# Optimization experiments

Measured on AMD Instinct MI355X. Metric: run time of the kernel, lower is better.

The kernel has to match this reference:

```python
import jax, jax.numpy as jnp
import numpy as np

N = 50000   # nodes
E = 640000  # edges (before self-loops)
D = 128     # in_channels = hidden_channels = out_channels
EPS_BN = 1e-5


def _gat(x, src, dst, W, a_src, a_dst, b, heads, concat):
    """PyG-style GATConv (self-loops already appended to src/dst)."""
    n = x.shape[0]
    C = W.shape[1] // heads
    xp = (x @ W).reshape(n, heads, C)                      # [N,H,C]
    asrc = jnp.sum(xp * a_src, -1)                          # [N,H]
    adst = jnp.sum(xp * a_dst, -1)                          # [N,H]
    e = jax.nn.leaky_relu(asrc[src] + adst[dst], 0.2)       # [Etot,H]
    m = jax.ops.segment_max(e, dst, num_segments=n)
    ex = jnp.exp(e - m[dst])
    s = jax.ops.segment_sum(ex, dst, num_segments=n)
    alpha = ex / (s[dst] + 1e-16)                           # segment softmax
    out = jax.ops.segment_sum(xp[src] * alpha[..., None], dst, num_segments=n)
    out = out.reshape(n, heads * C) if concat else out.mean(1)
    return out + b


def _gru(x, h, Wih, Whh, bih, bhh):
    gi = x @ Wih + bih
    gh = h @ Whh + bhh
    ir, iz, inn = jnp.split(gi, 3, -1)
    hr, hz, hn = jnp.split(gh, 3, -1)
    r = jax.nn.sigmoid(ir + hr)
    z = jax.nn.sigmoid(iz + hz)
    nn_ = jnp.tanh(inn + r * hn)
    return (1.0 - z) * nn_ + z * h


def setup_inputs() -> dict:
    key = jax.random.key(0)
    ks = jax.random.split(key, 32)
    f32 = jnp.float32
    p = lambda k, shape, s=0.1: jax.random.normal(k, shape, f32) * s
    inp = {
        "node_features": jax.random.normal(ks[0], (N, D), f32),
        "edge_index": jax.random.randint(ks[1], (2, E), 0, N),
        "x_prev1": jax.random.normal(ks[2], (N, D), f32),
        "x_prev2": jax.random.normal(ks[3], (N, D), f32),
        "ts": jax.random.uniform(ks[4], (N, 1), f32),
        # TimeEncode params
        "basis_freq": jnp.asarray(1.0 / 10 ** np.linspace(0, 9, D), f32),
        "phase": jnp.zeros((D,), f32),
        # MergeLayer: Linear(2D -> D)
        "merge_W": p(ks[5], (2 * D, D)),
        "merge_b": p(ks[6], (D,)),
        # layer1 GATConv(D -> D, heads=1, concat)
        "gat1_W": p(ks[7], (D, D)),
        "gat1_asrc": p(ks[8], (1, D)),
        "gat1_adst": p(ks[9], (1, D)),
        "gat1_b": p(ks[10], (D,)),
        # layer1 GRUCell(D, D)
        "gru1_Wih": p(ks[11], (D, 3 * D)),
        "gru1_Whh": p(ks[12], (D, 3 * D)),
        "gru1_bih": p(ks[13], (3 * D,)),
        "gru1_bhh": p(ks[14], (3 * D,)),
        # layer2 GATConv(D -> D, heads=1, concat=False)
        "gat2_W": p(ks[15], (D, D)),
        "gat2_asrc": p(ks[16], (1, D)),
        "gat2_adst": p(ks[17], (1, D)),
        "gat2_b": p(ks[18], (D,)),
        # layer2 GRUCell(D, D)
        "gru2_Wih": p(ks[19], (D, 3 * D)),
        "gru2_Whh": p(ks[20], (D, 3 * D)),
        "gru2_bih": p(ks[21], (3 * D,)),
        "gru2_bhh": p(ks[22], (3 * D,)),
        # skip connection Linear(D -> D)
        "skip_W": p(ks[23], (D, D)),
        "skip_b": p(ks[24], (D,)),
    }
    return inp


def reference(node_features, edge_index, x_prev1, x_prev2, ts,
              basis_freq, phase, merge_W, merge_b,
              gat1_W, gat1_asrc, gat1_adst, gat1_b,
              gru1_Wih, gru1_Whh, gru1_bih, gru1_bhh,
              gat2_W, gat2_asrc, gat2_adst, gat2_b,
              gru2_Wih, gru2_Whh, gru2_bih, gru2_bhh,
              skip_W, skip_b):
    n = node_features.shape[0]
    loop = jnp.arange(n)
    src = jnp.concatenate([edge_index[0], loop])  # add self-loops (PyG default)
    dst = jnp.concatenate([edge_index[1], loop])

    # TimeEncode: cos(ts * freq + phase) -> [N, D]
    t_embed = jnp.cos(ts * basis_freq[None, :] + phase[None, :])
    # MergeLayer
    x = jnp.concatenate([node_features, t_embed], -1) @ merge_W + merge_b

    # layer1: GAT + GRU, relu
    h1c = _gat(x, src, dst, gat1_W, gat1_asrc, gat1_adst, gat1_b, 1, True)
    H1 = jax.nn.relu(_gru(h1c, x_prev1, gru1_Wih, gru1_Whh, gru1_bih, gru1_bhh))

    # layer2: GAT + GRU + skip + fresh BatchNorm1d (training stats, identity affine)
    h2c = _gat(H1, src, dst, gat2_W, gat2_asrc, gat2_adst, gat2_b, 1, False)
    H2 = _gru(h2c, x_prev2, gru2_Wih, gru2_Whh, gru2_bih, gru2_bhh)
    H2 = H2 + (x @ skip_W + skip_b)
    mu = H2.mean(0)
    var = H2.var(0)
    H2 = (H2 - mu) / jnp.sqrt(var + EPS_BN)
    return (H1, H2)
```

## Files before the change

### kernel.cpp

```cpp
#include <hip/hip_runtime.h>
#include <math.h>

#define D 128
#define D3 384

typedef __attribute__((ext_vector_type(8))) short bf16x8;
typedef __attribute__((ext_vector_type(4))) float f32x4;
typedef __attribute__((ext_vector_type(4))) unsigned int u32x4;

__device__ __forceinline__ float fsigmoid(float x){
  return __builtin_amdgcn_rcpf(1.0f + __expf(-x));
}
__device__ __forceinline__ float ftanh(float x){
  float e = __expf(2.0f * x);
  return 1.0f - 2.0f * __builtin_amdgcn_rcpf(e + 1.0f);
}

__device__ __forceinline__ unsigned short f2bf(float f){
  unsigned u = __float_as_uint(f);
  return (unsigned short)((u + 0x7FFFu + ((u >> 16) & 1u)) >> 16);
}

__global__ __launch_bounds__(256) void k_init0(int* __restrict__ cnt, float* __restrict__ bns, int n){
  int idx = blockIdx.x * 256 + threadIdx.x;
  if (idx < n) cnt[idx] = 0;
  if (idx < 2 * D) bns[idx] = 0.0f;
}

__global__ __launch_bounds__(256) void k_wcvt(const float* __restrict__ W, unsigned short* __restrict__ Wt,
                                              int Nc, int K){
  int idx = blockIdx.x * 256 + threadIdx.x;
  if (idx >= K * Nc) return;
  int k = idx / Nc, c = idx - k * Nc;
  Wt[c * K + k] = f2bf(W[idx]);
}

__global__ __launch_bounds__(256) void k_merge(const float* __restrict__ nf, const float* __restrict__ ts,
                                               const float* __restrict__ freq, const float* __restrict__ phase,
                                               const unsigned short* __restrict__ Bt,
                                               const float* __restrict__ bias,
                                               unsigned short* __restrict__ xb, int M){
  __shared__ __align__(16) unsigned short Alds[64 * 256];
  const int tid = threadIdx.x;
  const int lane = tid & 63;
  const int w = tid >> 6;
  const int row0 = blockIdx.y * 64;

  #pragma unroll
  for (int r = 0; r < 8; ++r){
    int u = r * 256 + tid;
    int row = u >> 5, c16 = u & 31;
    int gr = row0 + row;
    union { unsigned short s[8]; bf16x8 v; } t;
    if (gr < M){
      if (c16 < 16){
        const float* p = nf + (size_t)gr * 128 + c16 * 8;
        float4 f0 = *(const float4*)p, f1 = *(const float4*)(p + 4);
        t.s[0]=f2bf(f0.x); t.s[1]=f2bf(f0.y); t.s[2]=f2bf(f0.z); t.s[3]=f2bf(f0.w);
        t.s[4]=f2bf(f1.x); t.s[5]=f2bf(f1.y); t.s[6]=f2bf(f1.z); t.s[7]=f2bf(f1.w);
      } else {
        float tv = ts[gr];
        int ch0 = (c16 - 16) * 8;
        float4 fq0 = *(const float4*)&freq[ch0],  fq1 = *(const float4*)&freq[ch0 + 4];
        float4 ph0 = *(const float4*)&phase[ch0], ph1 = *(const float4*)&phase[ch0 + 4];
        t.s[0]=f2bf(__cosf(tv*fq0.x+ph0.x)); t.s[1]=f2bf(__cosf(tv*fq0.y+ph0.y));
        t.s[2]=f2bf(__cosf(tv*fq0.z+ph0.z)); t.s[3]=f2bf(__cosf(tv*fq0.w+ph0.w));
        t.s[4]=f2bf(__cosf(tv*fq1.x+ph1.x)); t.s[5]=f2bf(__cosf(tv*fq1.y+ph1.y));
        t.s[6]=f2bf(__cosf(tv*fq1.z+ph1.z)); t.s[7]=f2bf(__cosf(tv*fq1.w+ph1.w));
      }
    } else {
      #pragma unroll
      for (int q = 0; q < 8; ++q) t.s[q] = 0;
    }
    int c16s = c16 ^ (row & 7);
    *(bf16x8*)&Alds[row * 256 + c16s * 8] = t.v;
  }
  __syncthreads();

  f32x4 acc[4][2];
  #pragma unroll
  for (int mf = 0; mf < 4; ++mf)
    #pragma unroll
    for (int nfi = 0; nfi < 2; ++nfi)
      #pragma unroll
      for (int i = 0; i < 4; ++i) acc[mf][nfi][i] = 0.0f;

  const int l15 = lane & 15, lg = lane >> 4;
  #pragma unroll
  for (int kk = 0; kk < 8; ++kk){
    const int c16 = kk * 4 + lg;
    bf16x8 a[4], b[2];
    #pragma unroll
    for (int nfi = 0; nfi < 2; ++nfi){
      int brow = w * 32 + nfi * 16 + l15;
      b[nfi] = *(const bf16x8*)&Bt[(size_t)brow * 256 + c16 * 8];
    }
    #pragma unroll
    for (int mf = 0; mf < 4; ++mf){
      int row = mf * 16 + l15;
      a[mf] = *(bf16x8*)&Alds[row * 256 + ((c16 ^ (row & 7))) * 8];
    }
    #pragma unroll
    for (int mf = 0; mf < 4; ++mf)
      #pragma unroll
      for (int nfi = 0; nfi < 2; ++nfi)
        acc[mf][nfi] = __builtin_amdgcn_mfma_f32_16x16x32_bf16(a[mf], b[nfi], acc[mf][nfi], 0, 0, 0);
  }

  #pragma unroll
  for (int nfi = 0; nfi < 2; ++nfi){
    int c = w * 32 + nfi * 16 + l15;
    float bv = bias[c];
    #pragma unroll
    for (int mf = 0; mf < 4; ++mf)
      #pragma unroll
      for (int i = 0; i < 4; ++i){
        int rr = row0 + mf * 16 + lg * 4 + i;
        if (rr < M) xb[(size_t)rr * 128 + c] = f2bf(acc[mf][nfi][i] + bv);
      }
  }
}

template<bool ABF16, bool OUTBF, bool ACCUM, bool BIAS>
__global__ __launch_bounds__(256) void k_mgemm(const void* __restrict__ Av,
                                               const unsigned short* __restrict__ Bt,
                                               const float* __restrict__ bias,
                                               void* __restrict__ Cv, int M, int Nc){
  __shared__ __align__(16) unsigned short Alds[64 * 128];
  const int tid = threadIdx.x;
  const int lane = tid & 63;
  const int w = tid >> 6;
  const int row0 = blockIdx.y * 64;
  const int col0 = blockIdx.x * 128;

  #pragma unroll
  for (int r = 0; r < 4; ++r){
    int u = r * 256 + tid;
    int row = u >> 4, c16 = u & 15;
    int gr = row0 + row;
    int c16s = c16 ^ (row & 7);
    if (ABF16){
      u32x4 v = {0,0,0,0};
      if (gr < M) v = *(const u32x4*)((const unsigned short*)Av + (size_t)gr * 128 + c16 * 8);
      *(u32x4*)&Alds[row * 128 + c16s * 8] = v;
    } else {
      float4 f0 = make_float4(0.f,0.f,0.f,0.f), f1 = f0;
      if (gr < M){
        const float* p = (const float*)Av + (size_t)gr * 128 + c16 * 8;
        f0 = *(const float4*)p; f1 = *(const float4*)(p + 4);
      }
      union { unsigned short s[8]; bf16x8 v; } t;
      t.s[0]=f2bf(f0.x); t.s[1]=f2bf(f0.y); t.s[2]=f2bf(f0.z); t.s[3]=f2bf(f0.w);
      t.s[4]=f2bf(f1.x); t.s[5]=f2bf(f1.y); t.s[6]=f2bf(f1.z); t.s[7]=f2bf(f1.w);
      *(bf16x8*)&Alds[row * 128 + c16s * 8] = t.v;
    }
  }
  __syncthreads();

  f32x4 acc[4][2];
  #pragma unroll
  for (int mf = 0; mf < 4; ++mf)
    #pragma unroll
    for (int nfi = 0; nfi < 2; ++nfi)
      #pragma unroll
      for (int i = 0; i < 4; ++i) acc[mf][nfi][i] = 0.0f;

  const int l15 = lane & 15, lg = lane >> 4;
  #pragma unroll
  for (int kk = 0; kk < 4; ++kk){
    const int c16 = kk * 4 + lg;
    bf16x8 a[4], b[2];
    #pragma unroll
    for (int nfi = 0; nfi < 2; ++nfi){
      int brow = col0 + w * 32 + nfi * 16 + l15;
      b[nfi] = *(const bf16x8*)&Bt[(size_t)brow * 128 + c16 * 8];
    }
    #pragma unroll
    for (int mf = 0; mf < 4; ++mf){
      int row = mf * 16 + l15;
      a[mf] = *(bf16x8*)&Alds[row * 128 + ((c16 ^ (row & 7))) * 8];
    }
    #pragma unroll
    for (int mf = 0; mf < 4; ++mf)
      #pragma unroll
      for (int nfi = 0; nfi < 2; ++nfi)
        acc[mf][nfi] = __builtin_amdgcn_mfma_f32_16x16x32_bf16(a[mf], b[nfi], acc[mf][nfi], 0, 0, 0);
  }

  #pragma unroll
  for (int nfi = 0; nfi < 2; ++nfi){
    int c = col0 + w * 32 + nfi * 16 + l15;
    float bv = BIAS ? bias[c] : 0.0f;
    #pragma unroll
    for (int mf = 0; mf < 4; ++mf)
      #pragma unroll
      for (int i = 0; i < 4; ++i){
        int rr = row0 + mf * 16 + lg * 4 + i;
        if (rr < M){
          size_t o = (size_t)rr * Nc + c;
          float v = acc[mf][nfi][i] + bv;
          if (OUTBF){
            ((unsigned short*)Cv)[o] = f2bf(v);
          } else {
            float* C = (float*)Cv;
            if (ACCUM) v += C[o];
            C[o] = v;
          }
        }
      }
  }
}

__global__ __launch_bounds__(256) void k_attn(const unsigned short* __restrict__ xpb,
                                              const float* __restrict__ a_s, const float* __restrict__ a_d,
                                              float* __restrict__ asrc, float* __restrict__ adst, int n){
  int wave = (blockIdx.x * 256 + threadIdx.x) >> 6;
  int lane = threadIdx.x & 63;
  if (wave >= n) return;
  unsigned u = *(const unsigned*)&xpb[(size_t)wave * D + 2 * lane];
  float lo = __uint_as_float(u << 16);
  float hi = __uint_as_float(u & 0xFFFF0000u);
  float2 as2 = *(const float2*)&a_s[2 * lane];
  float2 ad2 = *(const float2*)&a_d[2 * lane];
  float sa = lo * as2.x + hi * as2.y;
  float sd = lo * ad2.x + hi * ad2.y;
  #pragma unroll
  for (int off = 32; off > 0; off >>= 1){
    sa += __shfl_down(sa, off);
    sd += __shfl_down(sd, off);
  }
  if (lane == 0){ asrc[wave] = sa; adst[wave] = sd; }
}

__global__ __launch_bounds__(256) void k_hist(const int* __restrict__ ei, int* __restrict__ cnt, int e, int etot){
  int t = blockIdx.x * 256 + threadIdx.x;
  if (t >= etot) return;
  int d_ = (t < e) ? ei[e + t] : (t - e);
  atomicAdd(&cnt[d_], 1);
}

__global__ __launch_bounds__(256) void k_scan1(const int* __restrict__ cnt, int* __restrict__ off,
                                               int* __restrict__ bsum, int n){
  __shared__ int sm[256];
  int i = blockIdx.x * 256 + threadIdx.x;
  int v = (i < n) ? cnt[i] : 0;
  sm[threadIdx.x] = v;
  __syncthreads();
  #pragma unroll
  for (int d = 1; d < 256; d <<= 1){
    int t = (threadIdx.x >= d) ? sm[threadIdx.x - d] : 0;
    __syncthreads();
    sm[threadIdx.x] += t;
    __syncthreads();
  }
  if (i < n) off[i] = sm[threadIdx.x] - v;
  if (threadIdx.x == 255) bsum[blockIdx.x] = sm[255];
}

__global__ __launch_bounds__(256) void k_scan2(int* __restrict__ bsum, int nb){
  __shared__ int sm[256];
  int v = (threadIdx.x < nb) ? bsum[threadIdx.x] : 0;
  sm[threadIdx.x] = v;
  __syncthreads();
  #pragma unroll
  for (int d = 1; d < 256; d <<= 1){
    int t = (threadIdx.x >= d) ? sm[threadIdx.x - d] : 0;
    __syncthreads();
    sm[threadIdx.x] += t;
    __syncthreads();
  }
  if (threadIdx.x < nb) bsum[threadIdx.x] = sm[threadIdx.x] - v;
}

__global__ __launch_bounds__(256) void k_scan3(int* __restrict__ off, const int* __restrict__ bsum,
                                               int* __restrict__ cursor, int n, int etot){
  int i = blockIdx.x * 256 + threadIdx.x;
  if (i < n){
    int o = off[i] + bsum[blockIdx.x];
    off[i] = o;
    cursor[i] = o;
  }
  if (i == 0) off[n] = etot;
}

__global__ __launch_bounds__(256) void k_scatter(const int* __restrict__ ei, int* __restrict__ cursor,
                                                 int* __restrict__ csr, int e, int etot){
  int t = blockIdx.x * 256 + threadIdx.x;
  if (t >= etot) return;
  int s_, d_;
  if (t < e){ s_ = ei[t]; d_ = ei[e + t]; } else { s_ = d_ = t - e; }
  int pos = atomicAdd(&cursor[d_], 1);
  csr[pos] = s_;
}

__global__ __launch_bounds__(256) void k_gatconv(const int* __restrict__ off, const int* __restrict__ csr,
                                                 const float* __restrict__ asrc, const float* __restrict__ adst,
                                                 const unsigned short* __restrict__ xpb,
                                                 const float* __restrict__ bias,
                                                 unsigned short* __restrict__ outb, int n){
  int w = (blockIdx.x * 256 + threadIdx.x) >> 6;
  int lane = threadIdx.x & 63;
  if (w >= n) return;
  const int o0 = off[w], o1 = off[w + 1];
  const float ad = adst[w];
  float m = -1e30f;
  for (int j = o0 + lane; j < o1; j += 64){
    float v = asrc[csr[j]] + ad;
    v = (v > 0.0f) ? v : 0.2f * v;
    m = fmaxf(m, v);
  }
  #pragma unroll
  for (int d = 32; d > 0; d >>= 1) m = fmaxf(m, __shfl_xor(m, d));
  float s = 0.0f, acc0 = 0.0f, acc1 = 0.0f;
  for (int base = o0; base < o1; base += 64){
    int j = base + lane;
    float wgt = 0.0f;
    int src = 0;
    if (j < o1){
      src = csr[j];
      float v = asrc[src] + ad;
      v = (v > 0.0f) ? v : 0.2f * v;
      wgt = __expf(v - m);
    }
    s += wgt;
    const int cnt8 = (min(64, o1 - base) + 7) & ~7;
    const int wbits = __float_as_int(wgt);
    for (int t = 0; t < cnt8; t += 8){
      unsigned uu[8]; float wq[8];
      #pragma unroll
      for (int q = 0; q < 8; ++q){
        int sr = __builtin_amdgcn_readlane(src, t + q);
        wq[q] = __int_as_float(__builtin_amdgcn_readlane(wbits, t + q));
        uu[q] = *(const unsigned*)&xpb[(size_t)sr * D + 2 * lane];
      }
      #pragma unroll
      for (int q = 0; q < 8; ++q){
        acc0 = fmaf(wq[q], __uint_as_float(uu[q] << 16), acc0);
        acc1 = fmaf(wq[q], __uint_as_float(uu[q] & 0xFFFF0000u), acc1);
      }
    }
  }
  #pragma unroll
  for (int d = 32; d > 0; d >>= 1) s += __shfl_xor(s, d);
  float inv = 1.0f / (s + 1e-16f);
  float2 bv = *(const float2*)&bias[2 * lane];
  unsigned pack = ((unsigned)f2bf(acc1 * inv + bv.y) << 16) | f2bf(acc0 * inv + bv.x);
  *(unsigned*)&outb[(size_t)w * D + 2 * lane] = pack;
}

template<int RELU>
__global__ __launch_bounds__(512) void k_grugemm(const unsigned short* __restrict__ hgb,
                                                 const float* __restrict__ xprev,
                                                 const unsigned short* __restrict__ Wih,
                                                 const unsigned short* __restrict__ Whh,
                                                 const float* __restrict__ bih,
                                                 const float* __restrict__ bhh,
                                                 float* __restrict__ out, int n){
  __shared__ __align__(16) unsigned short A1lds[64 * 128];
  __shared__ __align__(16) unsigned short A2lds[64 * 128];
  const int tid = threadIdx.x;
  const int lane = tid & 63;
  const int w = tid >> 6;
  const int row0 = blockIdx.x * 64;

  #pragma unroll
  for (int r = 0; r < 2; ++r){
    int u = r * 512 + tid;
    int row = u >> 4, c16 = u & 15;
    int gr = row0 + row;
    int c16s = c16 ^ (row & 7);
    u32x4 v1 = {0,0,0,0};
    union { unsigned short s[8]; bf16x8 v; } t2;
    #pragma unroll
    for (int q = 0; q < 8; ++q) t2.s[q] = 0;
    if (gr < n){
      v1 = *(const u32x4*)(hgb + (size_t)gr * 128 + c16 * 8);
      const float* p = xprev + (size_t)gr * 128 + c16 * 8;
      float4 f0 = *(const float4*)p, f1 = *(const float4*)(p + 4);
      t2.s[0]=f2bf(f0.x); t2.s[1]=f2bf(f0.y); t2.s[2]=f2bf(f0.z); t2.s[3]=f2bf(f0.w);
      t2.s[4]=f2bf(f1.x); t2.s[5]=f2bf(f1.y); t2.s[6]=f2bf(f1.z); t2.s[7]=f2bf(f1.w);
    }
    *(u32x4*)&A1lds[row * 128 + c16s * 8] = v1;
    *(bf16x8*)&A2lds[row * 128 + c16s * 8] = t2.v;
  }
  __syncthreads();

  f32x4 accR[4], accZ[4], accN[4], accH[4];
  #pragma unroll
  for (int mf = 0; mf < 4; ++mf)
    #pragma unroll
    for (int i = 0; i < 4; ++i){ accR[mf][i]=0.f; accZ[mf][i]=0.f; accN[mf][i]=0.f; accH[mf][i]=0.f; }

  const int l15 = lane & 15, lg = lane >> 4;
  const int cw = w * 16 + l15;
  #pragma unroll
  for (int kk = 0; kk < 4; ++kk){
    const int c16 = kk * 4 + lg;
    bf16x8 a1[4], a2[4];
    #pragma unroll
    for (int mf = 0; mf < 4; ++mf){
      int row = mf * 16 + l15;
      int o = row * 128 + ((c16 ^ (row & 7))) * 8;
      a1[mf] = *(bf16x8*)&A1lds[o];
      a2[mf] = *(bf16x8*)&A2lds[o];
    }
    const size_t ko = (size_t)c16 * 8;
    bf16x8 bir = *(const bf16x8*)&Wih[(size_t)(cw      ) * 128 + ko];
    bf16x8 bhr = *(const bf16x8*)&Whh[(size_t)(cw      ) * 128 + ko];
    bf16x8 biz = *(const bf16x8*)&Wih[(size_t)(cw + 128) * 128 + ko];
    bf16x8 bhz = *(const bf16x8*)&Whh[(size_t)(cw + 128) * 128 + ko];
    bf16x8 bin = *(const bf16x8*)&Wih[(size_t)(cw + 256) * 128 + ko];
    bf16x8 bhn = *(const bf16x8*)&Whh[(size_t)(cw + 256) * 128 + ko];
    #pragma unroll
    for (int mf = 0; mf < 4; ++mf){
      accR[mf] = __builtin_amdgcn_mfma_f32_16x16x32_bf16(a1[mf], bir, accR[mf], 0, 0, 0);
      accR[mf] = __builtin_amdgcn_mfma_f32_16x16x32_bf16(a2[mf], bhr, accR[mf], 0, 0, 0);
      accZ[mf] = __builtin_amdgcn_mfma_f32_16x16x32_bf16(a1[mf], biz, accZ[mf], 0, 0, 0);
      accZ[mf] = __builtin_amdgcn_mfma_f32_16x16x32_bf16(a2[mf], bhz, accZ[mf], 0, 0, 0);
      accN[mf] = __builtin_amdgcn_mfma_f32_16x16x32_bf16(a1[mf], bin, accN[mf], 0, 0, 0);
      accH[mf] = __builtin_amdgcn_mfma_f32_16x16x32_bf16(a2[mf], bhn, accH[mf], 0, 0, 0);
    }
  }

  const float sbR = bih[cw] + bhh[cw];
  const float sbZ = bih[cw + 128] + bhh[cw + 128];
  const float biN = bih[cw + 256], bhN = bhh[cw + 256];
  #pragma unroll
  for (int mf = 0; mf < 4; ++mf)
    #pragma unroll
    for (int i = 0; i < 4; ++i){
      int rr = row0 + mf * 16 + lg * 4 + i;
      if (rr < n){
        float r  = fsigmoid(accR[mf][i] + sbR);
        float z  = fsigmoid(accZ[mf][i] + sbZ);
        float nn = ftanh(accN[mf][i] + biN + r * (accH[mf][i] + bhN));
        float hp = xprev[(size_t)rr * 128 + cw];
        float h = (1.0f - z) * nn + z * hp;
        if (RELU) h = fmaxf(h, 0.0f);
        out[(size_t)rr * 128 + cw] = h;
      }
    }
}

__global__ __launch_bounds__(256) void k_bnreduce(const float* __restrict__ H, float* __restrict__ bns, int n){
  int c = threadIdx.x & 127;
  int half = threadIdx.x >> 7;
  int r0 = blockIdx.x * 128;
  int rend = min(r0 + 128, n);
  float s0 = 0.0f, s1 = 0.0f;
  for (int r = r0 + half; r < rend; r += 2){
    float v = H[(size_t)r * D + c];
    s0 += v; s1 += v * v;
  }
  __shared__ float sm[2][128];
  if (half){ sm[0][c] = s0; sm[1][c] = s1; }
  __syncthreads();
  if (!half){
    s0 += sm[0][c]; s1 += sm[1][c];
    atomicAdd(&bns[c], s0);
    atomicAdd(&bns[D + c], s1);
  }
}

__global__ __launch_bounds__(256) void k_bnnorm(float* __restrict__ H, const float* __restrict__ bns, int n){
  int idx = blockIdx.x * 256 + threadIdx.x;
  if (idx >= n * D) return;
  int c = idx & 127;
  float inv_n = 1.0f / (float)n;
  float mu = bns[c] * inv_n;
  float var = bns[D + c] * inv_n - mu * mu;
  H[idx] = (H[idx] - mu) / sqrtf(var + 1e-5f);
}

extern "C" void kernel_launch(void* const* d_in, const int* in_sizes, int n_in,
                              void* d_out, int out_size, void* d_ws, size_t ws_size,
                              hipStream_t stream){
  const float* nf     = (const float*)d_in[0];
  const int*   ei     = (const int*)  d_in[1];
  const float* xprev[2] = { (const float*)d_in[2], (const float*)d_in[3] };
  const float* ts     = (const float*)d_in[4];
  const float* freq   = (const float*)d_in[5];
  const float* phase  = (const float*)d_in[6];
  const float* mergeW = (const float*)d_in[7];
  const float* mergeb = (const float*)d_in[8];
  const float* gatW[2]  = { (const float*)d_in[9],  (const float*)d_in[17] };
  const float* gatAS[2] = { (const float*)d_in[10], (const float*)d_in[18] };
  const float* gatAD[2] = { (const float*)d_in[11], (const float*)d_in[19] };
  const float* gatB[2]  = { (const float*)d_in[12], (const float*)d_in[20] };
  const float* Wih[2]   = { (const float*)d_in[13], (const float*)d_in[21] };
  const float* Whh[2]   = { (const float*)d_in[14], (const float*)d_in[22] };
  const float* bih[2]   = { (const float*)d_in[15], (const float*)d_in[23] };
  const float* bhh[2]   = { (const float*)d_in[16], (const float*)d_in[24] };
  const float* skipW  = (const float*)d_in[25];
  const float* skipb  = (const float*)d_in[26];

  const int n = in_sizes[0] / D;
  const int e = in_sizes[1] / 2;
  const int etot = e + n;
  const size_t nd = (size_t)n * D;

  float* ws   = (float*)d_ws;
  float* asrc = ws;
  float* adst = asrc + n;
  float* bns  = adst + n;
  int*   off  = (int*)(bns + 2 * D);
  int*   cnt  = off + n + 1;
  int*   bsum = cnt + n;
  int*   csr  = bsum + 256;
  unsigned short* WTm  = (unsigned short*)(csr + etot);
  unsigned short* WTg0 = WTm  + 32768;
  unsigned short* WTg1 = WTg0 + 16384;
  unsigned short* WTsk = WTg1 + 16384;
  unsigned short* WTih0 = WTsk + 16384;
  unsigned short* WThh0 = WTih0 + 49152;
  unsigned short* WTih1 = WThh0 + 49152;
  unsigned short* WThh1 = WTih1 + 49152;
  unsigned short* xb   = WThh1 + 49152;
  unsigned short* xpb  = xb  + nd;
  unsigned short* hgb  = xpb + nd;

  float* H1 = (float*)d_out;
  float* H2 = H1 + nd;

  const dim3 b256(256);
  const int nb_nd = (int)((nd + 255) / 256);
  const int nb_e  = (etot + 255) / 256;
  const int nb_n  = (n + 255) / 256;
  const int grows = (n + 63) / 64;
  const dim3 gm1(1, grows);
  const int gru_blocks = (n + 63) / 64;
  const int nb_wave = (int)(((size_t)n * 64 + 255) / 256);

  k_init0<<<nb_n, b256, 0, stream>>>(cnt, bns, n);
  k_hist<<<nb_e, b256, 0, stream>>>(ei, cnt, e, etot);
  k_scan1<<<nb_n, b256, 0, stream>>>(cnt, off, bsum, n);
  k_scan2<<<1, b256, 0, stream>>>(bsum, nb_n);
  k_scan3<<<nb_n, b256, 0, stream>>>(off, bsum, cnt, n, etot);
  k_scatter<<<nb_e, b256, 0, stream>>>(ei, cnt, csr, e, etot);

  k_wcvt<<<128, b256, 0, stream>>>(mergeW, WTm, 128, 256);
  k_wcvt<<< 64, b256, 0, stream>>>(gatW[0], WTg0, 128, 128);
  k_wcvt<<< 64, b256, 0, stream>>>(gatW[1], WTg1, 128, 128);
  k_wcvt<<< 64, b256, 0, stream>>>(skipW,   WTsk, 128, 128);
  k_wcvt<<<192, b256, 0, stream>>>(Wih[0], WTih0, 384, 128);
  k_wcvt<<<192, b256, 0, stream>>>(Whh[0], WThh0, 384, 128);
  k_wcvt<<<192, b256, 0, stream>>>(Wih[1], WTih1, 384, 128);
  k_wcvt<<<192, b256, 0, stream>>>(Whh[1], WThh1, 384, 128);

  k_merge<<<gm1, b256, 0, stream>>>(nf, ts, freq, phase, WTm, mergeb, xb, n);

  for (int L = 0; L < 2; ++L){
    float* gout = (L == 0) ? H1 : H2;
    const unsigned short* wtg  = (L == 0) ? WTg0 : WTg1;
    const unsigned short* wtih = (L == 0) ? WTih0 : WTih1;
    const unsigned short* wthh = (L == 0) ? WThh0 : WThh1;
    if (L == 0)
      k_mgemm<true , true, false, false><<<gm1, b256, 0, stream>>>(xb, wtg, nullptr, xpb, n, D);
    else
      k_mgemm<false, true, false, false><<<gm1, b256, 0, stream>>>(H1, wtg, nullptr, xpb, n, D);
    k_attn<<<nb_wave, b256, 0, stream>>>(xpb, gatAS[L], gatAD[L], asrc, adst, n);
    k_gatconv<<<nb_wave, b256, 0, stream>>>(off, csr, asrc, adst, xpb, gatB[L], hgb, n);
    if (L == 0)
      k_grugemm<1><<<gru_blocks, dim3(512), 0, stream>>>(hgb, xprev[0], wtih, wthh, bih[0], bhh[0], gout, n);
    else
      k_grugemm<0><<<gru_blocks, dim3(512), 0, stream>>>(hgb, xprev[1], wtih, wthh, bih[1], bhh[1], gout, n);
  }

  k_mgemm<true, false, true, true><<<gm1, b256, 0, stream>>>(xb, WTsk, skipb, H2, n, D);
  k_bnreduce<<<(n + 127) / 128, b256, 0, stream>>>(H2, bns, n);
  k_bnnorm<<<nb_nd, b256, 0, stream>>>(H2, bns, n);
}
```

Measured before the change: 507.7 us.

## Pre-pack weights into MFMA fragment order and merge conversion kernels

Weights are now converted once into a layout where each wave's B-fragment for a given k-step is a contiguous 512-element block indexed by lane, so global B loads become fully coalesced 16-byte-per-lane reads instead of strided row gathers. The eight separate weight-conversion launches are merged into one packing kernel. The LDS swizzle changes from XOR to an additive rotation of slots. This is meant to reduce weight-load traffic and latency in the GEMM and GRU kernels and to cut launch overhead, at the cost of more complex index maths in the packing step.

```diff
diff --git a/kernel.cpp b/kernel.cpp
--- a/kernel.cpp
+++ b/kernel.cpp
@@ -20,6 +20,9 @@
   unsigned u = __float_as_uint(f);
   return (unsigned short)((u + 0x7FFFu + ((u >> 16) & 1u)) >> 16);
 }
+
+__device__ __forceinline__ int slot16(int c, int row){ return (c + 2 * (row & 7)) & 15; }
+__device__ __forceinline__ int slot32(int c, int row){ return (c + 2 * (row & 7)) & 31; }
 
 __global__ __launch_bounds__(256) void k_init0(int* __restrict__ cnt, float* __restrict__ bns, int n){
   int idx = blockIdx.x * 256 + threadIdx.x;
@@ -27,17 +30,42 @@
   if (idx < 2 * D) bns[idx] = 0.0f;
 }
 
-__global__ __launch_bounds__(256) void k_wcvt(const float* __restrict__ W, unsigned short* __restrict__ Wt,
-                                              int Nc, int K){
+__global__ __launch_bounds__(256) void k_wpackall(
+    const float* __restrict__ mergeW, const float* __restrict__ g0, const float* __restrict__ g1,
+    const float* __restrict__ sk, const float* __restrict__ ih0, const float* __restrict__ hh0,
+    const float* __restrict__ ih1, const float* __restrict__ hh1,
+    unsigned short* __restrict__ Pm, unsigned short* __restrict__ Pg0, unsigned short* __restrict__ Pg1,
+    unsigned short* __restrict__ Psk, unsigned short* __restrict__ Pu0, unsigned short* __restrict__ Pu1){
   int idx = blockIdx.x * 256 + threadIdx.x;
-  if (idx >= K * Nc) return;
-  int k = idx / Nc, c = idx - k * Nc;
-  Wt[c * K + k] = f2bf(W[idx]);
+  if (idx < 32768){
+    int i = idx;
+    int j = i & 7, l15 = (i >> 3) & 15, lg = (i >> 7) & 3, nf = (i >> 9) & 1, kk = (i >> 10) & 7, w = (i >> 13) & 3;
+    int col = w * 32 + nf * 16 + l15, k = (kk * 4 + lg) * 8 + j;
+    Pm[i] = f2bf(mergeW[k * 128 + col]);
+  } else if (idx < 81920){
+    int seg = (idx - 32768) >> 14;
+    int i = (idx - 32768) & 16383;
+    const float* W = seg == 0 ? g0 : (seg == 1 ? g1 : sk);
+    unsigned short* P = seg == 0 ? Pg0 : (seg == 1 ? Pg1 : Psk);
+    int j = i & 7, l15 = (i >> 3) & 15, lg = (i >> 7) & 3, nf = (i >> 9) & 1, kk = (i >> 10) & 3, w = (i >> 12) & 3;
+    int col = w * 32 + nf * 16 + l15, k = (kk * 4 + lg) * 8 + j;
+    P[i] = f2bf(W[k * 128 + col]);
+  } else if (idx < 278528){
+    int seg = (idx - 81920) / 98304;
+    int i = (idx - 81920) % 98304;
+    const float* Wih = seg ? ih1 : ih0;
+    const float* Whh = seg ? hh1 : hh0;
+    unsigned short* P = seg ? Pu1 : Pu0;
+    int j = i & 7, l15 = (i >> 3) & 15, lg = (i >> 7) & 3;
+    int r9 = i >> 9; int t = r9 % 6; int r = r9 / 6; int kk = r & 3, w = r >> 2;
+    int col = (t >> 1) * 128 + w * 16 + l15, k = (kk * 4 + lg) * 8 + j;
+    P[i] = f2bf((t & 1 ? Whh : Wih)[k * 384 + col]);
+  }
 }
 
 __global__ __launch_bounds__(256) void k_merge(const float* __restrict__ nf, const float* __restrict__ ts,
                                                const float* __restrict__ freq, const float* __restrict__ phase,
-                                               const unsigned short* __restrict__ Bt,
+                                               const unsigned short* __restrict__ Pm,
                                                const float* __restrict__ bias,
                                                unsigned short* __restrict__ xb, int M){
   __shared__ __align__(16) unsigned short Alds[64 * 256];
@@ -72,8 +100,7 @@
       #pragma unroll
       for (int q = 0; q < 8; ++q) t.s[q] = 0;
     }
-    int c16s = c16 ^ (row & 7);
-    *(bf16x8*)&Alds[row * 256 + c16s * 8] = t.v;
+    *(bf16x8*)&Alds[row * 256 + slot32(c16, row) * 8] = t.v;
   }
   __syncthreads();
 
@@ -91,14 +118,12 @@
     const int c16 = kk * 4 + lg;
     bf16x8 a[4], b[2];
     #pragma unroll
-    for (int nfi = 0; nfi < 2; ++nfi){
-      int brow = w * 32 + nfi * 16 + l15;
-      b[nfi] = *(const bf16x8*)&Bt[(size_t)brow * 256 + c16 * 8];
-    }
+    for (int nfi = 0; nfi < 2; ++nfi)
+      b[nfi] = *(const bf16x8*)&Pm[(size_t)((w * 8 + kk) * 2 + nfi) * 512 + lane * 8];
     #pragma unroll
     for (int mf = 0; mf < 4; ++mf){
       int row = mf * 16 + l15;
-      a[mf] = *(bf16x8*)&Alds[row * 256 + ((c16 ^ (row & 7))) * 8];
+      a[mf] = *(bf16x8*)&Alds[row * 256 + slot32(c16, row) * 8];
     }
     #pragma unroll
     for (int mf = 0; mf < 4; ++mf)
@@ -123,22 +148,21 @@
 
 template<bool ABF16, bool OUTBF, bool ACCUM, bool BIAS>
 __global__ __launch_bounds__(256) void k_mgemm(const void* __restrict__ Av,
-                                               const unsigned short* __restrict__ Bt,
+                                               const unsigned short* __restrict__ Pg,
                                                const float* __restrict__ bias,
-                                               void* __restrict__ Cv, int M, int Nc){
+                                               void* __restrict__ Cv, int M){
   __shared__ __align__(16) unsigned short Alds[64 * 128];
   const int tid = threadIdx.x;
   const int lane = tid & 63;
   const int w = tid >> 6;
   const int row0 = blockIdx.y * 64;
-  const int col0 = blockIdx.x * 128;
 
   #pragma unroll
   for (int r = 0; r < 4; ++r){
     int u = r * 256 + tid;
     int row = u >> 4, c16 = u & 15;
     int gr = row0 + row;
-    int c16s = c16 ^ (row & 7);
+    int c16s = slot16(c16, row);
     if (ABF16){
       u32x4 v = {0,0,0,0};
       if (gr < M) v = *(const u32x4*)((const unsigned short*)Av + (size_t)gr * 128 + c16 * 8);
@@ -171,14 +195,12 @@
     const int c16 = kk * 4 + lg;
     bf16x8 a[4], b[2];
     #pragma unroll
-    for (int nfi = 0; nfi < 2; ++nfi){
-      int brow = col0 + w * 32 + nfi * 16 + l15;
-      b[nfi] = *(const bf16x8*)&Bt[(size_t)brow * 128 + c16 * 8];
-    }
+    for (int nfi = 0; nfi < 2; ++nfi)
+      b[nfi] = *(const bf16x8*)&Pg[(size_t)((w * 4 + kk) * 2 + nfi) * 512 + lane * 8];
     #pragma unroll
     for (int mf = 0; mf < 4; ++mf){
       int row = mf * 16 + l15;
-      a[mf] = *(bf16x8*)&Alds[row * 128 + ((c16 ^ (row & 7))) * 8];
+      a[mf] = *(bf16x8*)&Alds[row * 128 + slot16(c16, row) * 8];
     }
     #pragma unroll
     for (int mf = 0; mf < 4; ++mf)
@@ -189,7 +211,7 @@
 
   #pragma unroll
   for (int nfi = 0; nfi < 2; ++nfi){
-    int c = col0 + w * 32 + nfi * 16 + l15;
+    int c = w * 32 + nfi * 16 + l15;
     float bv = BIAS ? bias[c] : 0.0f;
     #pragma unroll
     for (int mf = 0; mf < 4; ++mf)
@@ -197,7 +219,7 @@
       for (int i = 0; i < 4; ++i){
         int rr = row0 + mf * 16 + lg * 4 + i;
         if (rr < M){
-          size_t o = (size_t)rr * Nc + c;
+          size_t o = (size_t)rr * 128 + c;
           float v = acc[mf][nfi][i] + bv;
           if (OUTBF){
             ((unsigned short*)Cv)[o] = f2bf(v);
@@ -351,8 +373,7 @@
 template<int RELU>
 __global__ __launch_bounds__(512) void k_grugemm(const unsigned short* __restrict__ hgb,
                                                  const float* __restrict__ xprev,
-                                                 const unsigned short* __restrict__ Wih,
-                                                 const unsigned short* __restrict__ Whh,
+                                                 const unsigned short* __restrict__ Pu,
                                                  const float* __restrict__ bih,
                                                  const float* __restrict__ bhh,
                                                  float* __restrict__ out, int n){
@@ -368,7 +389,7 @@
     int u = r * 512 + tid;
     int row = u >> 4, c16 = u & 15;
     int gr = row0 + row;
-    int c16s = c16 ^ (row & 7);
+    int c16s = slot16(c16, row);
     u32x4 v1 = {0,0,0,0};
     union { unsigned short s[8]; bf16x8 v; } t2;
     #pragma unroll
@@ -396,21 +417,21 @@
   #pragma unroll
   for (int kk = 0; kk < 4; ++kk){
     const int c16 = kk * 4 + lg;
+    const unsigned short* Pb = Pu + (size_t)(w * 4 + kk) * 3072 + lane * 8;
+    bf16x8 bir = *(const bf16x8*)&Pb[0];
+    bf16x8 bhr = *(const bf16x8*)&Pb[512];
+    bf16x8 biz = *(const bf16x8*)&Pb[1024];
+    bf16x8 bhz = *(const bf16x8*)&Pb[1536];
+    bf16x8 bin = *(const bf16x8*)&Pb[2048];
+    bf16x8 bhn = *(const bf16x8*)&Pb[2560];
     bf16x8 a1[4], a2[4];
     #pragma unroll
     for (int mf = 0; mf < 4; ++mf){
       int row = mf * 16 + l15;
-      int o = row * 128 + ((c16 ^ (row & 7))) * 8;
+      int o = row * 128 + slot16(c16, row) * 8;
       a1[mf] = *(bf16x8*)&A1lds[o];
       a2[mf] = *(bf16x8*)&A2lds[o];
     }
-    const size_t ko = (size_t)c16 * 8;
-    bf16x8 bir = *(const bf16x8*)&Wih[(size_t)(cw      ) * 128 + ko];
-    bf16x8 bhr = *(const bf16x8*)&Whh[(size_t)(cw      ) * 128 + ko];
-    bf16x8 biz = *(const bf16x8*)&Wih[(size_t)(cw + 128) * 128 + ko];
-    bf16x8 bhz = *(const bf16x8*)&Whh[(size_t)(cw + 128) * 128 + ko];
-    bf16x8 bin = *(const bf16x8*)&Wih[(size_t)(cw + 256) * 128 + ko];
-    bf16x8 bhn = *(const bf16x8*)&Whh[(size_t)(cw + 256) * 128 + ko];
     #pragma unroll
     for (int mf = 0; mf < 4; ++mf){
       accR[mf] = __builtin_amdgcn_mfma_f32_16x16x32_bf16(a1[mf], bir, accR[mf], 0, 0, 0);
@@ -507,17 +528,16 @@
   int*   cnt  = off + n + 1;
   int*   bsum = cnt + n;
   int*   csr  = bsum + 256;
-  unsigned short* WTm  = (unsigned short*)(csr + etot);
-  unsigned short* WTg0 = WTm  + 32768;
-  unsigned short* WTg1 = WTg0 + 16384;
-  unsigned short* WTsk = WTg1 + 16384;
-  unsigned short* WTih0 = WTsk + 16384;
-  unsigned short* WThh0 = WTih0 + 49152;
-  unsigned short* WTih1 = WThh0 + 49152;
-  unsigned short* WThh1 = WTih1 + 49152;
-  unsigned short* xb   = WThh1 + 49152;
-  unsigned short* xpb  = xb  + nd;
-  unsigned short* hgb  = xpb + nd;
+  uintptr_t pa = ((uintptr_t)(csr + etot) + 15) & ~(uintptr_t)15;
+  unsigned short* Pm  = (unsigned short*)pa;
+  unsigned short* Pg0 = Pm  + 32768;
+  unsigned short* Pg1 = Pg0 + 16384;
+  unsigned short* Psk = Pg1 + 16384;
+  unsigned short* Pu0 = Psk + 16384;
+  unsigned short* Pu1 = Pu0 + 98304;
+  unsigned short* xb  = Pu1 + 98304;
+  unsigned short* xpb = xb  + nd;
+  unsigned short* hgb = xpb + nd;
 
   float* H1 = (float*)d_out;
   float* H2 = H1 + nd;
@@ -538,35 +558,29 @@
   k_scan3<<<nb_n, b256, 0, stream>>>(off, bsum, cnt, n, etot);
   k_scatter<<<nb_e, b256, 0, stream>>>(ei, cnt, csr, e, etot);
 
-  k_wcvt<<<128, b256, 0, stream>>>(mergeW, WTm, 128, 256);
-  k_wcvt<<< 64, b256, 0, stream>>>(gatW[0], WTg0, 128, 128);
-  k_wcvt<<< 64, b256, 0, stream>>>(gatW[1], WTg1, 128, 128);
-  k_wcvt<<< 64, b256, 0, stream>>>(skipW,   WTsk, 128, 128);
-  k_wcvt<<<192, b256, 0, stream>>>(Wih[0], WTih0, 384, 128);
-  k_wcvt<<<192, b256, 0, stream>>>(Whh[0], WThh0, 384, 128);
-  k_wcvt<<<192, b256, 0, stream>>>(Wih[1], WTih1, 384, 128);
-  k_wcvt<<<192, b256, 0, stream>>>(Whh[1], WThh1, 384, 128);
-
-  k_merge<<<gm1, b256, 0, stream>>>(nf, ts, freq, phase, WTm, mergeb, xb, n);
+  k_wpackall<<<(278528 + 255) / 256, b256, 0, stream>>>(
+      mergeW, gatW[0], gatW[1], skipW, Wih[0], Whh[0], Wih[1], Whh[1],
+      Pm, Pg0, Pg1, Psk, Pu0, Pu1);
+
+  k_merge<<<gm1, b256, 0, stream>>>(nf, ts, freq, phase, Pm, mergeb, xb, n);
 
   for (int L = 0; L < 2; ++L){
     float* gout = (L == 0) ? H1 : H2;
-    const unsigned short* wtg  = (L == 0) ? WTg0 : WTg1;
-    const unsigned short* wtih = (L == 0) ? WTih0 : WTih1;
-    const unsigned short* wthh = (L == 0) ? WThh0 : WThh1;
+    const unsigned short* wtg = (L == 0) ? Pg0 : Pg1;
+    const unsigned short* pu  = (L == 0) ? Pu0 : Pu1;
     if (L == 0)
-      k_mgemm<true , true, false, false><<<gm1, b256, 0, stream>>>(xb, wtg, nullptr, xpb, n, D);
+      k_mgemm<true , true, false, false><<<gm1, b256, 0, stream>>>(xb, wtg, nullptr, xpb, n);
     else
-      k_mgemm<false, true, false, false><<<gm1, b256, 0, stream>>>(H1, wtg, nullptr, xpb, n, D);
+      k_mgemm<false, true, false, false><<<gm1, b256, 0, stream>>>(H1, wtg, nullptr, xpb, n);
     k_attn<<<nb_wave, b256, 0, stream>>>(xpb, gatAS[L], gatAD[L], asrc, adst, n);
     k_gatconv<<<nb_wave, b256, 0, stream>>>(off, csr, asrc, adst, xpb, gatB[L], hgb, n);
     if (L == 0)
-      k_grugemm<1><<<gru_blocks, dim3(512), 0, stream>>>(hgb, xprev[0], wtih, wthh, bih[0], bhh[0], gout, n);
+      k_grugemm<1><<<gru_blocks, dim3(512), 0, stream>>>(hgb, xprev[0], pu, bih[0], bhh[0], gout, n);
     else
-      k_grugemm<0><<<gru_blocks, dim3(512), 0, stream>>>(hgb, xprev[1], wtih, wthh, bih[1], bhh[1], gout, n);
-  }
-
-  k_mgemm<true, false, true, true><<<gm1, b256, 0, stream>>>(xb, WTsk, skipb, H2, n, D);
+      k_grugemm<0><<<gru_blocks, dim3(512), 0, stream>>>(hgb, xprev[1], pu, bih[1], bhh[1], gout, n);
+  }
+
+  k_mgemm<true, false, true, true><<<gm1, b256, 0, stream>>>(xb, Psk, skipb, H2, n);
   k_bnreduce<<<(n + 127) / 128, b256, 0, stream>>>(H2, bns, n);
   k_bnnorm<<<nb_nd, b256, 0, stream>>>(H2, bns, n);
 }
```

After: 461.7 us. 9.1% less time.
